# Performance work log

Hardware: AMD Instinct MI355X
Metric: run time of the kernel (lower is better)

Reference implementation:

```python
import jax, jax.numpy as jnp
import numpy as np

BETA = 0.2


def setup_inputs() -> dict:
    key = jax.random.key(0)
    ks = jax.random.split(key, 9)
    B, IN, W, OUT = 1024, 256, 512, 1
    def init_w(k, o, i):
        # torch.nn.Linear default: U(-1/sqrt(in), 1/sqrt(in))
        bound = 1.0 / np.sqrt(i)
        return jax.random.uniform(k, (o, i), jnp.float32, -bound, bound)
    def init_b(k, o, i):
        bound = 1.0 / np.sqrt(i)
        return jax.random.uniform(k, (o,), jnp.float32, -bound, bound)
    return {
        "x":  jax.random.normal(ks[0], (B, IN), jnp.float32),
        "W1": init_w(ks[1], W, IN),  "b1": init_b(ks[2], W, IN),
        "W2": init_w(ks[3], W, W),   "b2": init_b(ks[4], W, W),
        "W3": init_w(ks[5], W, W),   "b3": init_b(ks[6], W, W),
        "W4": init_w(ks[7], OUT, W), "b4": init_b(ks[8], OUT, W),
    }


def _max_tempered_out(x, W, b, beta=BETA):
    # lineared: standard linear part, (B, out)
    lin = jnp.einsum('oi,bi->bo', W, x)
    # tropical part: max over input dim of elementwise weight*input, (B, out)
    mx = jnp.max(W[None, :, :] * x[:, None, :], axis=-1)
    return (1.0 - beta) * lin + beta * mx + b


def reference(x, W1, b1, W2, b2, W3, b3, W4, b4):
    h = _max_tempered_out(x, W1, b1)
    h = _max_tempered_out(h, W2, b2)
    h = _max_tempered_out(h, W3, b3)
    out = _max_tempered_out(h, W4, b4)
    return jnp.squeeze(out, axis=-1)  # output_width == 1 -> (B,)
```

## Files before the change

kernel.cpp:

```cpp
#include <hip/hip_runtime.h>
#include <math.h>


#define NT   512
#define ROWS 4

typedef float v2f __attribute__((ext_vector_type(2)));
typedef float v4f __attribute__((ext_vector_type(4)));

#define V2LO(v) __builtin_shufflevector((v), (v), 0, 1)
#define V2HI(v) __builtin_shufflevector((v), (v), 2, 3)

#define WT1_OFF 0
#define WT2_OFF 33280
#define WT3_OFF 99328

__global__ __launch_bounds__(256) void transpose_all(
    const float* __restrict__ W1, const float* __restrict__ W2,
    const float* __restrict__ W3, float4* __restrict__ ws)
{
    const int tid = blockIdx.x * 256 + threadIdx.x;
    const float* W;
    float4* WT;
    int o, k4, K;
    if (tid < 32768) {
        W = W1; WT = ws + WT1_OFF; K = 256;
        o = tid >> 6; k4 = tid & 63;
    } else if (tid < 98304) {
        const int idx = tid - 32768;
        W = W2; WT = ws + WT2_OFF; K = 512;
        o = idx >> 7; k4 = idx & 127;
    } else {
        const int idx = tid - 98304;
        W = W3; WT = ws + WT3_OFF; K = 512;
        o = idx >> 7; k4 = idx & 127;
    }
    float4 v = *(const float4*)&W[(size_t)o * K + 4 * k4];
    WT[(size_t)k4 * 512 + o] = v;
}

#define COMPUTE_KG(W0, W1, W2, W3, KB)                                      \
    {                                                                       \
        _Pragma("unroll")                                                   \
        for (int j = 0; j < 4; ++j) {                                       \
            const v4f w = (j == 0) ? (W0) : (j == 1) ? (W1)                 \
                        : (j == 2) ? (W2) : (W3);                           \
            const v2f wL = V2LO(w), wH = V2HI(w);                           \
            const int k = ((KB) + j) * 4;                                   \
            _Pragma("unroll")                                               \
            for (int r = 0; r < ROWS; ++r) {                                \
                const v4f h = *(const v4f*)&hin[r][k];                      \
                const v2f hL = V2LO(h), hH = V2HI(h);                       \
                v2f pL = wL * hL;                                           \
                v2f pH = wH * hH;                                           \
                sL[r] += pL;                                                \
                sH[r] += pH;                                                \
                mL[r] = fmaxf(fmaxf(mL[r], pL[0]), pL[1]);                  \
                mH[r] = fmaxf(fmaxf(mH[r], pH[0]), pH[1]);                  \
            }                                                               \
        }                                                                   \
    }

__device__ __forceinline__ void layer_bcast(
    const float (*__restrict__ hin)[512],
    float (*__restrict__ hout)[512],
    const v4f* __restrict__ WT,
    const float* __restrict__ bias,
    int K4, int t)
{
    v2f sL[ROWS], sH[ROWS];
    float mL[ROWS], mH[ROWS];
    #pragma unroll
    for (int r = 0; r < ROWS; ++r) {
        sL[r] = (v2f)0.f; sH[r] = (v2f)0.f;
        mL[r] = -INFINITY; mH[r] = -INFINITY;
    }

    const v4f* wp = WT + t;

    v4f a0 = wp[0],    a1 = wp[512],  a2 = wp[1024], a3 = wp[1536];
    v4f b0 = wp[2048], b1 = wp[2560], b2 = wp[3072], b3 = wp[3584];

    for (int kg = 0; kg < K4; kg += 8) {
        v4f ta0 = a0, ta1 = a1, ta2 = a2, ta3 = a3;
        if (kg + 8 < K4) {
            const v4f* q = wp + (size_t)(kg + 8) * 512;
            ta0 = q[0]; ta1 = q[512]; ta2 = q[1024]; ta3 = q[1536];
        }
        COMPUTE_KG(a0, a1, a2, a3, kg);
        a0 = ta0; a1 = ta1; a2 = ta2; a3 = ta3;

        v4f tb0 = b0, tb1 = b1, tb2 = b2, tb3 = b3;
        if (kg + 12 < K4) {
            const v4f* q = wp + (size_t)(kg + 12) * 512;
            tb0 = q[0]; tb1 = q[512]; tb2 = q[1024]; tb3 = q[1536];
        }
        COMPUTE_KG(b0, b1, b2, b3, kg + 4);
        b0 = tb0; b1 = tb1; b2 = tb2; b3 = tb3;
    }

    const float bo = bias[t];
    #pragma unroll
    for (int r = 0; r < ROWS; ++r) {
        v2f sv = sL[r] + sH[r];
        float s = sv[0] + sv[1];
        float m = fmaxf(mL[r], mH[r]);
        hout[r][t] = fmaf(0.2f, m, fmaf(0.8f, s, bo));
    }
}

__global__ __launch_bounds__(NT) void net_fused(
    const float* __restrict__ x,
    const v4f* __restrict__ WT1, const float* __restrict__ b1,
    const v4f* __restrict__ WT2, const float* __restrict__ b2,
    const v4f* __restrict__ WT3, const float* __restrict__ b3,
    const float* __restrict__ W4, const float* __restrict__ b4,
    float* __restrict__ out)
{
    __shared__ __align__(16) float ha[ROWS][512];
    __shared__ __align__(16) float hb[ROWS][512];
    __shared__ float red_s[8][ROWS];
    __shared__ float red_m[8][ROWS];

    const int t = threadIdx.x;
    const int row0 = blockIdx.x * ROWS;

    {
        const int r = t >> 7;
        const int c = (t & 127) * 2;
        float2 v = *(const float2*)&x[(size_t)(row0 + r) * 256 + c];
        ha[r][c]     = v.x;
        ha[r][c + 1] = v.y;
    }
    __syncthreads();

    layer_bcast(ha, hb, WT1, b1, 64,  t);
    __syncthreads();
    layer_bcast(hb, ha, WT2, b2, 128, t);
    __syncthreads();
    layer_bcast(ha, hb, WT3, b3, 128, t);
    __syncthreads();

    const float w4 = W4[t];
    float ps[ROWS], pm[ROWS];
    #pragma unroll
    for (int r = 0; r < ROWS; ++r) {
        float p = w4 * hb[r][t];
        ps[r] = p;
        pm[r] = p;
    }
    #pragma unroll
    for (int off = 32; off; off >>= 1) {
        #pragma unroll
        for (int r = 0; r < ROWS; ++r) {
            ps[r] += __shfl_xor(ps[r], off, 64);
            pm[r] = fmaxf(pm[r], __shfl_xor(pm[r], off, 64));
        }
    }
    const int lane = t & 63;
    const int wave = t >> 6;
    if (lane == 0) {
        #pragma unroll
        for (int r = 0; r < ROWS; ++r) {
            red_s[wave][r] = ps[r];
            red_m[wave][r] = pm[r];
        }
    }
    __syncthreads();

    if (t < ROWS) {
        float s = red_s[0][t];
        float m = red_m[0][t];
        #pragma unroll
        for (int w = 1; w < 8; ++w) {
            s += red_s[w][t];
            m = fmaxf(m, red_m[w][t]);
        }
        out[row0 + t] = fmaf(0.2f, m, fmaf(0.8f, s, b4[0]));
    }
}

extern "C" void kernel_launch(void* const* d_in, const int* in_sizes, int n_in,
                              void* d_out, int out_size, void* d_ws, size_t ws_size,
                              hipStream_t stream)
{
    const float* x  = (const float*)d_in[0];
    const float* W1 = (const float*)d_in[1];
    const float* b1 = (const float*)d_in[2];
    const float* W2 = (const float*)d_in[3];
    const float* b2 = (const float*)d_in[4];
    const float* W3 = (const float*)d_in[5];
    const float* b3 = (const float*)d_in[6];
    const float* W4 = (const float*)d_in[7];
    const float* b4 = (const float*)d_in[8];

    float4* ws4 = (float4*)d_ws;

    transpose_all<<<640, 256, 0, stream>>>(W1, W2, W3, ws4);

    net_fused<<<256, NT, 0, stream>>>(
        x,
        (const v4f*)(ws4 + WT1_OFF), b1,
        (const v4f*)(ws4 + WT2_OFF), b2,
        (const v4f*)(ws4 + WT3_OFF), b3,
        W4, b4,
        (float*)d_out);
}
```

Measured before the change: 62.81 us.

## Remap threads to 2 rows x 2 outputs per thread in fused MLP layers

Replaces the one-output-per-thread, four-rows mapping with a register tile of two rows by two output columns per thread. Each wave handles a row pair and a 64-wide output stripe, so every thread now loads two weight vectors and two activation vectors per k-step. The inner loop is also rewritten as a software-pipelined, non-unrolled loop with v4f products and split max accumulators. This changes the ratio of LDS reads to global weight reads and lowers register pressure from the heavy unroll, at the cost of each weight column being read by two waves (one per row pair).

```diff
diff --git a/kernel.cpp b/kernel.cpp
--- a/kernel.cpp
+++ b/kernel.cpp
@@ -3,13 +3,9 @@
 
 
 #define NT   512
-#define ROWS 4
 
 typedef float v2f __attribute__((ext_vector_type(2)));
 typedef float v4f __attribute__((ext_vector_type(4)));
-
-#define V2LO(v) __builtin_shufflevector((v), (v), 0, 1)
-#define V2HI(v) __builtin_shufflevector((v), (v), 2, 3)
 
 #define WT1_OFF 0
 #define WT2_OFF 33280
@@ -39,73 +35,90 @@
     WT[(size_t)k4 * 512 + o] = v;
 }
 
-#define COMPUTE_KG(W0, W1, W2, W3, KB)                                      \
+#define STEP(WL, WH, H0, H1)                                                \
     {                                                                       \
-        _Pragma("unroll")                                                   \
-        for (int j = 0; j < 4; ++j) {                                       \
-            const v4f w = (j == 0) ? (W0) : (j == 1) ? (W1)                 \
-                        : (j == 2) ? (W2) : (W3);                           \
-            const v2f wL = V2LO(w), wH = V2HI(w);                           \
-            const int k = ((KB) + j) * 4;                                   \
-            _Pragma("unroll")                                               \
-            for (int r = 0; r < ROWS; ++r) {                                \
-                const v4f h = *(const v4f*)&hin[r][k];                      \
-                const v2f hL = V2LO(h), hH = V2HI(h);                       \
-                v2f pL = wL * hL;                                           \
-                v2f pH = wH * hH;                                           \
-                sL[r] += pL;                                                \
-                sH[r] += pH;                                                \
-                mL[r] = fmaxf(fmaxf(mL[r], pL[0]), pL[1]);                  \
-                mH[r] = fmaxf(fmaxf(mH[r], pH[0]), pH[1]);                  \
-            }                                                               \
-        }                                                                   \
-    }
-
-__device__ __forceinline__ void layer_bcast(
+        v4f p;                                                              \
+        p = (WL) * (H0); sl0 += p;                                          \
+        ml0a = fmaxf(fmaxf(ml0a, p[0]), p[1]);                              \
+        ml0b = fmaxf(fmaxf(ml0b, p[2]), p[3]);                              \
+        p = (WL) * (H1); sl1 += p;                                          \
+        ml1a = fmaxf(fmaxf(ml1a, p[0]), p[1]);                              \
+        ml1b = fmaxf(fmaxf(ml1b, p[2]), p[3]);                              \
+        p = (WH) * (H0); sh0 += p;                                          \
+        mh0a = fmaxf(fmaxf(mh0a, p[0]), p[1]);                              \
+        mh0b = fmaxf(fmaxf(mh0b, p[2]), p[3]);                              \
+        p = (WH) * (H1); sh1 += p;                                          \
+        mh1a = fmaxf(fmaxf(mh1a, p[0]), p[1]);                              \
+        mh1b = fmaxf(fmaxf(mh1b, p[2]), p[3]);                              \
+    }
+
+template<int K4>
+__device__ __forceinline__ void layer_gr(
     const float (*__restrict__ hin)[512],
     float (*__restrict__ hout)[512],
     const v4f* __restrict__ WT,
     const float* __restrict__ bias,
-    int K4, int t)
-{
-    v2f sL[ROWS], sH[ROWS];
-    float mL[ROWS], mH[ROWS];
-    #pragma unroll
-    for (int r = 0; r < ROWS; ++r) {
-        sL[r] = (v2f)0.f; sH[r] = (v2f)0.f;
-        mL[r] = -INFINITY; mH[r] = -INFINITY;
-    }
-
-    const v4f* wp = WT + t;
-
-    v4f a0 = wp[0],    a1 = wp[512],  a2 = wp[1024], a3 = wp[1536];
-    v4f b0 = wp[2048], b1 = wp[2560], b2 = wp[3072], b3 = wp[3584];
-
-    for (int kg = 0; kg < K4; kg += 8) {
-        v4f ta0 = a0, ta1 = a1, ta2 = a2, ta3 = a3;
-        if (kg + 8 < K4) {
-            const v4f* q = wp + (size_t)(kg + 8) * 512;
-            ta0 = q[0]; ta1 = q[512]; ta2 = q[1024]; ta3 = q[1536];
-        }
-        COMPUTE_KG(a0, a1, a2, a3, kg);
-        a0 = ta0; a1 = ta1; a2 = ta2; a3 = ta3;
-
-        v4f tb0 = b0, tb1 = b1, tb2 = b2, tb3 = b3;
-        if (kg + 12 < K4) {
-            const v4f* q = wp + (size_t)(kg + 12) * 512;
-            tb0 = q[0]; tb1 = q[512]; tb2 = q[1024]; tb3 = q[1536];
-        }
-        COMPUTE_KG(b0, b1, b2, b3, kg + 4);
-        b0 = tb0; b1 = tb1; b2 = tb2; b3 = tb3;
-    }
-
-    const float bo = bias[t];
-    #pragma unroll
-    for (int r = 0; r < ROWS; ++r) {
-        v2f sv = sL[r] + sH[r];
-        float s = sv[0] + sv[1];
-        float m = fmaxf(mL[r], mH[r]);
-        hout[r][t] = fmaf(0.2f, m, fmaf(0.8f, s, bo));
+    int rp, int o_lo)
+{
+    const v4f* wpl = WT + o_lo;
+    const v4f* wph = wpl + 64;
+    const v4f* h0p = (const v4f*)hin[2 * rp];
+    const v4f* h1p = (const v4f*)hin[2 * rp + 1];
+
+    v4f sl0 = (v4f)0.f, sl1 = (v4f)0.f, sh0 = (v4f)0.f, sh1 = (v4f)0.f;
+    float ml0a = -INFINITY, ml0b = -INFINITY, ml1a = -INFINITY, ml1b = -INFINITY;
+    float mh0a = -INFINITY, mh0b = -INFINITY, mh1a = -INFINITY, mh1b = -INFINITY;
+
+    v4f wl0 = wpl[0 * 512], wh0 = wph[0 * 512];
+    v4f wl1 = wpl[1 * 512], wh1 = wph[1 * 512];
+    v4f wl2 = wpl[2 * 512], wh2 = wph[2 * 512];
+    v4f wl3 = wpl[3 * 512], wh3 = wph[3 * 512];
+    v4f h00 = h0p[0], h01 = h1p[0];
+    v4f h10 = h0p[1], h11 = h1p[1];
+    v4f h20 = h0p[2], h21 = h1p[2];
+    v4f h30 = h0p[3], h31 = h1p[3];
+
+    #pragma unroll 1
+    for (int kg = 0; kg + 4 < K4; kg += 4) {
+        STEP(wl0, wh0, h00, h01);
+        wl0 = wpl[(size_t)(kg + 4) * 512]; wh0 = wph[(size_t)(kg + 4) * 512];
+        h00 = h0p[kg + 4]; h01 = h1p[kg + 4];
+        STEP(wl1, wh1, h10, h11);
+        wl1 = wpl[(size_t)(kg + 5) * 512]; wh1 = wph[(size_t)(kg + 5) * 512];
+        h10 = h0p[kg + 5]; h11 = h1p[kg + 5];
+        STEP(wl2, wh2, h20, h21);
+        wl2 = wpl[(size_t)(kg + 6) * 512]; wh2 = wph[(size_t)(kg + 6) * 512];
+        h20 = h0p[kg + 6]; h21 = h1p[kg + 6];
+        STEP(wl3, wh3, h30, h31);
+        wl3 = wpl[(size_t)(kg + 7) * 512]; wh3 = wph[(size_t)(kg + 7) * 512];
+        h30 = h0p[kg + 7]; h31 = h1p[kg + 7];
+    }
+    STEP(wl0, wh0, h00, h01);
+    STEP(wl1, wh1, h10, h11);
+    STEP(wl2, wh2, h20, h21);
+    STEP(wl3, wh3, h30, h31);
+
+    const float blo = bias[o_lo];
+    const float bhi = bias[o_lo + 64];
+    {
+        float s = (sl0[0] + sl0[1]) + (sl0[2] + sl0[3]);
+        hout[2 * rp][o_lo] =
+            fmaf(0.2f, fmaxf(ml0a, ml0b), fmaf(0.8f, s, blo));
+    }
+    {
+        float s = (sl1[0] + sl1[1]) + (sl1[2] + sl1[3]);
+        hout[2 * rp + 1][o_lo] =
+            fmaf(0.2f, fmaxf(ml1a, ml1b), fmaf(0.8f, s, blo));
+    }
+    {
+        float s = (sh0[0] + sh0[1]) + (sh0[2] + sh0[3]);
+        hout[2 * rp][o_lo + 64] =
+            fmaf(0.2f, fmaxf(mh0a, mh0b), fmaf(0.8f, s, bhi));
+    }
+    {
+        float s = (sh1[0] + sh1[1]) + (sh1[2] + sh1[3]);
+        hout[2 * rp + 1][o_lo + 64] =
+            fmaf(0.2f, fmaxf(mh1a, mh1b), fmaf(0.8f, s, bhi));
     }
 }
 
@@ -117,13 +130,13 @@
     const float* __restrict__ W4, const float* __restrict__ b4,
     float* __restrict__ out)
 {
-    __shared__ __align__(16) float ha[ROWS][512];
-    __shared__ __align__(16) float hb[ROWS][512];
-    __shared__ float red_s[8][ROWS];
-    __shared__ float red_m[8][ROWS];
+    __shared__ __align__(16) float ha[4][512];
+    __shared__ __align__(16) float hb[4][512];
+    __shared__ float red_s[8][4];
+    __shared__ float red_m[8][4];
 
     const int t = threadIdx.x;
-    const int row0 = blockIdx.x * ROWS;
+    const int row0 = blockIdx.x * 4;
 
     {
         const int r = t >> 7;
@@ -134,41 +147,46 @@
     }
     __syncthreads();
 
-    layer_bcast(ha, hb, WT1, b1, 64,  t);
-    __syncthreads();
-    layer_bcast(hb, ha, WT2, b2, 128, t);
-    __syncthreads();
-    layer_bcast(ha, hb, WT3, b3, 128, t);
+    const int wave = t >> 6;
+    const int lane = t & 63;
+    const int rp   = wave & 1;
+    const int o_lo = (wave >> 1) * 128 + lane;
+
+    layer_gr<64> (ha, hb, WT1, b1, rp, o_lo);
+    __syncthreads();
+    layer_gr<128>(hb, ha, WT2, b2, rp, o_lo);
+    __syncthreads();
+    layer_gr<128>(ha, hb, WT3, b3, rp, o_lo);
     __syncthreads();
 
     const float w4 = W4[t];
-    float ps[ROWS], pm[ROWS];
-    #pragma unroll
-    for (int r = 0; r < ROWS; ++r) {
-        float p = w4 * hb[r][t];
-        ps[r] = p;
-        pm[r] = p;
+    float ps0, ps1, ps2, ps3, pm0, pm1, pm2, pm3;
+    {
+        float p0 = w4 * hb[0][t]; ps0 = p0; pm0 = p0;
+        float p1 = w4 * hb[1][t]; ps1 = p1; pm1 = p1;
+        float p2 = w4 * hb[2][t]; ps2 = p2; pm2 = p2;
+        float p3 = w4 * hb[3][t]; ps3 = p3; pm3 = p3;
     }
     #pragma unroll
     for (int off = 32; off; off >>= 1) {
-        #pragma unroll
-        for (int r = 0; r < ROWS; ++r) {
-            ps[r] += __shfl_xor(ps[r], off, 64);
-            pm[r] = fmaxf(pm[r], __shfl_xor(pm[r], off, 64));
-        }
-    }
-    const int lane = t & 63;
-    const int wave = t >> 6;
+        ps0 += __shfl_xor(ps0, off, 64);
+        pm0 = fmaxf(pm0, __shfl_xor(pm0, off, 64));
+        ps1 += __shfl_xor(ps1, off, 64);
+        pm1 = fmaxf(pm1, __shfl_xor(pm1, off, 64));
+        ps2 += __shfl_xor(ps2, off, 64);
+        pm2 = fmaxf(pm2, __shfl_xor(pm2, off, 64));
+        ps3 += __shfl_xor(ps3, off, 64);
+        pm3 = fmaxf(pm3, __shfl_xor(pm3, off, 64));
+    }
     if (lane == 0) {
-        #pragma unroll
-        for (int r = 0; r < ROWS; ++r) {
-            red_s[wave][r] = ps[r];
-            red_m[wave][r] = pm[r];
-        }
-    }
-    __syncthreads();
-
-    if (t < ROWS) {
+        red_s[wave][0] = ps0; red_m[wave][0] = pm0;
+        red_s[wave][1] = ps1; red_m[wave][1] = pm1;
+        red_s[wave][2] = ps2; red_m[wave][2] = pm2;
+        red_s[wave][3] = ps3; red_m[wave][3] = pm3;
+    }
+    __syncthreads();
+
+    if (t < 4) {
         float s = red_s[0][t];
         float m = red_m[0][t];
         #pragma unroll
```

Result: no change. 62.05 us (-1.2%).

## Halve rows per block to launch more blocks and register-pipeline h loads

Applied to the files above, without the earlier changes.

Each block now processes 2 batch rows instead of 4, doubling the grid to 512 blocks so more of the GPU's compute units are occupied. The inner loop is rewritten with hand-unrolled per-k4 steps that software-pipeline both the transposed weight loads and the LDS activation loads in registers. The trade-off is that each weight element is now reused across fewer rows, which doubles total weight traffic from L2/global memory.

```diff
diff --git a/kernel.cpp b/kernel.cpp
--- a/kernel.cpp
+++ b/kernel.cpp
@@ -3,7 +3,7 @@
 
 
 #define NT   512
-#define ROWS 4
+#define ROWS 2
 
 typedef float v2f __attribute__((ext_vector_type(2)));
 typedef float v4f __attribute__((ext_vector_type(4)));
@@ -39,26 +39,17 @@
     WT[(size_t)k4 * 512 + o] = v;
 }
 
-#define COMPUTE_KG(W0, W1, W2, W3, KB)                                      \
+#define K4_STEP(wv, H0, H1)                                                 \
     {                                                                       \
-        _Pragma("unroll")                                                   \
-        for (int j = 0; j < 4; ++j) {                                       \
-            const v4f w = (j == 0) ? (W0) : (j == 1) ? (W1)                 \
-                        : (j == 2) ? (W2) : (W3);                           \
-            const v2f wL = V2LO(w), wH = V2HI(w);                           \
-            const int k = ((KB) + j) * 4;                                   \
-            _Pragma("unroll")                                               \
-            for (int r = 0; r < ROWS; ++r) {                                \
-                const v4f h = *(const v4f*)&hin[r][k];                      \
-                const v2f hL = V2LO(h), hH = V2HI(h);                       \
-                v2f pL = wL * hL;                                           \
-                v2f pH = wH * hH;                                           \
-                sL[r] += pL;                                                \
-                sH[r] += pH;                                                \
-                mL[r] = fmaxf(fmaxf(mL[r], pL[0]), pL[1]);                  \
-                mH[r] = fmaxf(fmaxf(mH[r], pH[0]), pH[1]);                  \
-            }                                                               \
-        }                                                                   \
+        const v2f wLo = V2LO(wv), wHi = V2HI(wv);                           \
+        { v2f pL = V2LO(H0) * wLo, pH = V2HI(H0) * wHi;                     \
+          sL0 += pL; sH0 += pH;                                             \
+          mL0 = fmaxf(fmaxf(mL0, pL[0]), pL[1]);                            \
+          mH0 = fmaxf(fmaxf(mH0, pH[0]), pH[1]); }                          \
+        { v2f pL = V2LO(H1) * wLo, pH = V2HI(H1) * wHi;                     \
+          sL1 += pL; sH1 += pH;                                             \
+          mL1 = fmaxf(fmaxf(mL1, pL[0]), pL[1]);                            \
+          mH1 = fmaxf(fmaxf(mH1, pH[0]), pH[1]); }                          \
     }
 
 __device__ __forceinline__ void layer_bcast(
@@ -68,44 +59,47 @@
     const float* __restrict__ bias,
     int K4, int t)
 {
-    v2f sL[ROWS], sH[ROWS];
-    float mL[ROWS], mH[ROWS];
-    #pragma unroll
-    for (int r = 0; r < ROWS; ++r) {
-        sL[r] = (v2f)0.f; sH[r] = (v2f)0.f;
-        mL[r] = -INFINITY; mH[r] = -INFINITY;
-    }
+    v2f sL0 = (v2f)0.f, sH0 = (v2f)0.f, sL1 = (v2f)0.f, sH1 = (v2f)0.f;
+    float mL0 = -INFINITY, mH0 = -INFINITY, mL1 = -INFINITY, mH1 = -INFINITY;
 
     const v4f* wp = WT + t;
+    const v4f* h0p = (const v4f*)hin[0];
+    const v4f* h1p = (const v4f*)hin[1];
 
-    v4f a0 = wp[0],    a1 = wp[512],  a2 = wp[1024], a3 = wp[1536];
-    v4f b0 = wp[2048], b1 = wp[2560], b2 = wp[3072], b3 = wp[3584];
+    v4f w0 = wp[0], w1 = wp[512], w2 = wp[1024], w3 = wp[1536];
+    v4f h00 = h0p[0], h01 = h1p[0];
+    v4f h10 = h0p[1], h11 = h1p[1];
+    v4f h20 = h0p[2], h21 = h1p[2];
+    v4f h30 = h0p[3], h31 = h1p[3];
 
-    for (int kg = 0; kg < K4; kg += 8) {
-        v4f ta0 = a0, ta1 = a1, ta2 = a2, ta3 = a3;
-        if (kg + 8 < K4) {
-            const v4f* q = wp + (size_t)(kg + 8) * 512;
-            ta0 = q[0]; ta1 = q[512]; ta2 = q[1024]; ta3 = q[1536];
-        }
-        COMPUTE_KG(a0, a1, a2, a3, kg);
-        a0 = ta0; a1 = ta1; a2 = ta2; a3 = ta3;
-
-        v4f tb0 = b0, tb1 = b1, tb2 = b2, tb3 = b3;
-        if (kg + 12 < K4) {
-            const v4f* q = wp + (size_t)(kg + 12) * 512;
-            tb0 = q[0]; tb1 = q[512]; tb2 = q[1024]; tb3 = q[1536];
-        }
-        COMPUTE_KG(b0, b1, b2, b3, kg + 4);
-        b0 = tb0; b1 = tb1; b2 = tb2; b3 = tb3;
+    #pragma unroll 1
+    for (int kg = 0; kg + 4 < K4; kg += 4) {
+        K4_STEP(w0, h00, h01);
+        w0 = wp[(size_t)(kg + 4) * 512];
+        h00 = h0p[kg + 4]; h01 = h1p[kg + 4];
+        K4_STEP(w1, h10, h11);
+        w1 = wp[(size_t)(kg + 5) * 512];
+        h10 = h0p[kg + 5]; h11 = h1p[kg + 5];
+        K4_STEP(w2, h20, h21);
+        w2 = wp[(size_t)(kg + 6) * 512];
+        h20 = h0p[kg + 6]; h21 = h1p[kg + 6];
+        K4_STEP(w3, h30, h31);
+        w3 = wp[(size_t)(kg + 7) * 512];
+        h30 = h0p[kg + 7]; h31 = h1p[kg + 7];
     }
+    K4_STEP(w0, h00, h01);
+    K4_STEP(w1, h10, h11);
+    K4_STEP(w2, h20, h21);
+    K4_STEP(w3, h30, h31);
 
     const float bo = bias[t];
-    #pragma unroll
-    for (int r = 0; r < ROWS; ++r) {
-        v2f sv = sL[r] + sH[r];
-        float s = sv[0] + sv[1];
-        float m = fmaxf(mL[r], mH[r]);
-        hout[r][t] = fmaf(0.2f, m, fmaf(0.8f, s, bo));
+    {
+        v2f sv = sL0 + sH0;
+        hout[0][t] = fmaf(0.2f, fmaxf(mL0, mH0), fmaf(0.8f, sv[0] + sv[1], bo));
+    }
+    {
+        v2f sv = sL1 + sH1;
+        hout[1][t] = fmaf(0.2f, fmaxf(mL1, mH1), fmaf(0.8f, sv[0] + sv[1], bo));
     }
 }
 
@@ -126,11 +120,9 @@
     const int row0 = blockIdx.x * ROWS;
 
     {
-        const int r = t >> 7;
-        const int c = (t & 127) * 2;
-        float2 v = *(const float2*)&x[(size_t)(row0 + r) * 256 + c];
-        ha[r][c]     = v.x;
-        ha[r][c + 1] = v.y;
+        const int r = t >> 8;
+        const int c = t & 255;
+        ha[r][c] = x[(size_t)(row0 + r) * 256 + c];
     }
     __syncthreads();
 
@@ -142,29 +134,23 @@
     __syncthreads();
 
     const float w4 = W4[t];
-    float ps[ROWS], pm[ROWS];
-    #pragma unroll
-    for (int r = 0; r < ROWS; ++r) {
-        float p = w4 * hb[r][t];
-        ps[r] = p;
-        pm[r] = p;
+    float ps0, ps1, pm0, pm1;
+    {
+        float p0 = w4 * hb[0][t]; ps0 = p0; pm0 = p0;
+        float p1 = w4 * hb[1][t]; ps1 = p1; pm1 = p1;
     }
     #pragma unroll
     for (int off = 32; off; off >>= 1) {
-        #pragma unroll
-        for (int r = 0; r < ROWS; ++r) {
-            ps[r] += __shfl_xor(ps[r], off, 64);
-            pm[r] = fmaxf(pm[r], __shfl_xor(pm[r], off, 64));
-        }
+        ps0 += __shfl_xor(ps0, off, 64);
+        pm0 = fmaxf(pm0, __shfl_xor(pm0, off, 64));
+        ps1 += __shfl_xor(ps1, off, 64);
+        pm1 = fmaxf(pm1, __shfl_xor(pm1, off, 64));
     }
     const int lane = t & 63;
     const int wave = t >> 6;
     if (lane == 0) {
-        #pragma unroll
-        for (int r = 0; r < ROWS; ++r) {
-            red_s[wave][r] = ps[r];
-            red_m[wave][r] = pm[r];
-        }
+        red_s[wave][0] = ps0; red_m[wave][0] = pm0;
+        red_s[wave][1] = ps1; red_m[wave][1] = pm1;
     }
     __syncthreads();
 
@@ -198,7 +184,7 @@
 
     transpose_all<<<640, 256, 0, stream>>>(W1, W2, W3, ws4);
 
-    net_fused<<<256, NT, 0, stream>>>(
+    net_fused<<<512, NT, 0, stream>>>(
         x,
         (const v4f*)(ws4 + WT1_OFF), b1,
         (const v4f*)(ws4 + WT2_OFF), b2,
```

Result: slower. 67.02 us (+6.7%).
